# Kernel tuning notes

Hardware: AMD Instinct MI355X
Metric: run time of the kernel (lower is better)

The kernel has to match this reference:

```python
import jax, jax.numpy as jnp
import numpy as np

N = 100000   # nodes
E = 3200000  # edges
B = 64       # graphs in batch
NUM_CLASSES = 40


def _linear_params(key, out_c, in_c):
    k1, k2 = jax.random.split(key)
    bound = 1.0 / np.sqrt(in_c)
    W = jax.random.uniform(k1, (out_c, in_c), jnp.float32, -bound, bound)
    b = jax.random.uniform(k2, (out_c,), jnp.float32, -bound, bound)
    return W, b


def setup_inputs() -> dict:
    key = jax.random.key(0)
    ks = jax.random.split(key, 8)
    pos = jax.random.normal(ks[0], (N, 3), jnp.float32)
    edge_index = jax.random.randint(ks[1], (2, E), 0, N, dtype=jnp.int64)
    batch = jnp.sort(jax.random.randint(ks[2], (N,), 0, B, dtype=jnp.int64))
    # conv1 mlp: Linear(3+3 -> 32), Linear(32 -> 32)
    W11, b11 = _linear_params(ks[3], 32, 6)
    W12, b12 = _linear_params(ks[4], 32, 32)
    # conv2 mlp: Linear(32+3 -> 32), Linear(32 -> 32)
    W21, b21 = _linear_params(ks[5], 32, 35)
    W22, b22 = _linear_params(ks[6], 32, 32)
    # classifier: Linear(32 -> num_classes)
    Wc, bc = _linear_params(ks[7], NUM_CLASSES, 32)
    return {"pos": pos, "edge_index": edge_index, "batch": batch,
            "W11": W11, "b11": b11, "W12": W12, "b12": b12,
            "W21": W21, "b21": b21, "W22": W22, "b22": b22,
            "Wc": Wc, "bc": bc}


def _pointnet_layer(h, pos, src, dst, W1, b1, W2, b2):
    # message: concat(h_j, pos_j - pos_i) -> Linear -> ReLU -> Linear  per edge
    edge_feat = jnp.concatenate([h[src], pos[src] - pos[dst]], axis=-1)  # [E, C+3]
    m = jax.nn.relu(edge_feat @ W1.T + b1) @ W2.T + b2                   # [E, out]
    # aggr='max': scatter-max into target nodes; empty nodes -> 0
    agg = jax.ops.segment_max(m, dst, num_segments=N)
    return jnp.where(jnp.isneginf(agg), 0.0, agg)


def reference(pos, edge_index, batch, W11, b11, W12, b12, W21, b21, W22, b22, Wc, bc):
    src, dst = edge_index[0], edge_index[1]  # j (source), i (target)
    h = _pointnet_layer(pos, pos, src, dst, W11, b11, W12, b12)
    h = jax.nn.relu(h)
    h = _pointnet_layer(h, pos, src, dst, W21, b21, W22, b22)
    h = jax.nn.relu(h)
    g = jax.ops.segment_max(h, batch, num_segments=B)  # global_max_pool -> [B, 32]
    g = jnp.where(jnp.isneginf(g), 0.0, g)
    return g @ Wc.T + bc  # [B, num_classes]
```

## Files before the change

kernel.cpp:

```cpp
#include <hip/hip_runtime.h>

#define N_NODES 100000
#define N_EDGES 3200000
#define N_B 64
#define N_CLS 40
#define SCAN_NBLK 98
#define CAP 96

__global__ __launch_bounds__(256) void node1_kernel(
    const float* __restrict__ pos, const float* __restrict__ W11,
    const float* __restrict__ b11, float* __restrict__ A, float* __restrict__ C) {
  int n = blockIdx.x * 256 + threadIdx.x;
  if (n >= N_NODES) return;
  float p0 = pos[n * 3 + 0], p1 = pos[n * 3 + 1], p2 = pos[n * 3 + 2];
#pragma unroll
  for (int c = 0; c < 32; ++c) {
    float wa0 = W11[c * 6 + 0], wa1 = W11[c * 6 + 1], wa2 = W11[c * 6 + 2];
    float wp0 = W11[c * 6 + 3], wp1 = W11[c * 6 + 4], wp2 = W11[c * 6 + 5];
    float cp = p0 * wp0 + p1 * wp1 + p2 * wp2;
    A[(size_t)n * 32 + c] = p0 * wa0 + p1 * wa1 + p2 * wa2 + cp + b11[c];
    C[(size_t)n * 32 + c] = -cp;
  }
}

__global__ __launch_bounds__(256) void node2_kernel(
    const float* __restrict__ h1, const float* __restrict__ pos,
    const float* __restrict__ W21, const float* __restrict__ b21,
    float* __restrict__ A, float* __restrict__ C) {
  __shared__ float Wl[32 * 35];
  __shared__ float bl[32];
  for (int i = threadIdx.x; i < 32 * 35; i += 256) Wl[i] = W21[i];
  if (threadIdx.x < 32) bl[threadIdx.x] = b21[threadIdx.x];
  __syncthreads();

  int n = blockIdx.x * 256 + threadIdx.x;
  if (n >= N_NODES) return;

  float h[32];
  const float4* hp = reinterpret_cast<const float4*>(h1 + (size_t)n * 32);
#pragma unroll
  for (int q = 0; q < 8; ++q) {
    float4 v = hp[q];
    h[4 * q + 0] = v.x; h[4 * q + 1] = v.y;
    h[4 * q + 2] = v.z; h[4 * q + 3] = v.w;
  }
  float p0 = pos[n * 3 + 0], p1 = pos[n * 3 + 1], p2 = pos[n * 3 + 2];
#pragma unroll 4
  for (int co = 0; co < 32; ++co) {
    const float* wr = Wl + co * 35;
    float acc = bl[co];
#pragma unroll
    for (int k = 0; k < 32; ++k) acc = fmaf(h[k], wr[k], acc);
    float cp = p0 * wr[32] + p1 * wr[33] + p2 * wr[34];
    A[(size_t)n * 32 + co] = acc + cp;
    C[(size_t)n * 32 + co] = -cp;
  }
}

__global__ __launch_bounds__(256) void pscatter_kernel(
    const int* __restrict__ ei, int* __restrict__ cnt, int* __restrict__ slot) {
  int e = blockIdx.x * 256 + threadIdx.x;
  int s = ei[e];
  int d = ei[N_EDGES + e];
  int p = atomicAdd(cnt + d, 1);
  if (p < CAP) slot[d * CAP + p] = s;
}

__global__ __launch_bounds__(1024) void scan1_kernel(
    const int* __restrict__ cnt, int* __restrict__ offsets,
    int* __restrict__ bsum) {
  __shared__ int wsum[16];
  int i = blockIdx.x * 1024 + threadIdx.x;
  int lane = threadIdx.x & 63, wid = threadIdx.x >> 6;
  int v = (i < N_NODES) ? cnt[i] : 0;
  int x = v;
#pragma unroll
  for (int off = 1; off < 64; off <<= 1) {
    int t = __shfl_up(x, off, 64);
    if (lane >= off) x += t;
  }
  if (lane == 63) wsum[wid] = x;
  __syncthreads();
  if (wid == 0) {
    int s = (lane < 16) ? wsum[lane] : 0;
#pragma unroll
    for (int off = 1; off < 16; off <<= 1) {
      int t = __shfl_up(s, off, 64);
      if (lane >= off) s += t;
    }
    if (lane < 16) wsum[lane] = s;
  }
  __syncthreads();
  int excl = x - v + ((wid > 0) ? wsum[wid - 1] : 0);
  if (i < N_NODES) offsets[i] = excl;
  if (threadIdx.x == 0) bsum[blockIdx.x] = wsum[15];
}

__global__ __launch_bounds__(128) void scan2_kernel(int* __restrict__ bsum) {
  __shared__ int wtot[2];
  int i = threadIdx.x;
  int lane = i & 63, wid = i >> 6;
  int v = (i < SCAN_NBLK) ? bsum[i] : 0;
  int x = v;
#pragma unroll
  for (int off = 1; off < 64; off <<= 1) {
    int t = __shfl_up(x, off, 64);
    if (lane >= off) x += t;
  }
  if (lane == 63) wtot[wid] = x;
  __syncthreads();
  int excl = x - v + ((wid > 0) ? wtot[0] : 0);
  if (i < SCAN_NBLK) bsum[i] = excl;
}

__global__ __launch_bounds__(1024) void scan3_kernel(
    int* __restrict__ offsets, const int* __restrict__ bsum) {
  int i = blockIdx.x * 1024 + threadIdx.x;
  if (i < N_NODES) offsets[i] += bsum[blockIdx.x];
  if (blockIdx.x == 0 && threadIdx.x == 0) offsets[N_NODES] = N_EDGES;
}

__global__ __launch_bounds__(256) void compact_kernel(
    const int* __restrict__ offsets, const int* __restrict__ slot,
    int* __restrict__ ssrc, int* __restrict__ sdst) {
  int n = blockIdx.x * 256 + threadIdx.x;
  if (n >= N_NODES) return;
  int j0 = offsets[n];
  int deg = offsets[n + 1] - j0;
  if (deg > CAP) deg = CAP;
  const int* sp = slot + (size_t)n * CAP;
  for (int j = 0; j < deg; ++j) {
    ssrc[j0 + j] = sp[j];
    sdst[j0 + j] = n;
  }
}

__global__ __launch_bounds__(256) void edge_mlp_kernel(
    const int* __restrict__ ssrc, const int* __restrict__ sdst,
    const float* __restrict__ A, const float* __restrict__ C,
    const float* __restrict__ W2, const float* __restrict__ b2,
    unsigned* __restrict__ h) {
  __shared__ float Tm[256 * 33];
  __shared__ float Wl[1024];
  __shared__ float bl32[32];
  __shared__ short segstart[258];
  __shared__ int segdst[256];
  __shared__ int wh[4];
  __shared__ int nseg_s;

  int t = threadIdx.x;
  for (int i = t; i < 1024; i += 256) Wl[i] = W2[i];
  if (t < 32) bl32[t] = b2[t];

  int e = blockIdx.x * 256 + t;
  int s = ssrc[e];
  int d = sdst[e];
  int dprev = (e > 0) ? sdst[e - 1] : -1;
  bool head = (t == 0) || (d != dprev);

  unsigned long long mask = __ballot(head);
  int lane = t & 63, wid = t >> 6;
  if (lane == 63) wh[wid] = __popcll(mask);
  __syncthreads();
  int base = 0;
#pragma unroll
  for (int w = 0; w < 3; ++w) base += (w < wid) ? wh[w] : 0;
  int segid = base + __popcll(mask & ((2ULL << lane) - 1)) - 1;
  if (head) { segstart[segid] = (short)t; segdst[segid] = d; }
  if (t == 255) { nseg_s = segid + 1; segstart[segid + 1] = 256; }

  float r[32];
  const float4* Ap = reinterpret_cast<const float4*>(A + (size_t)s * 32);
  const float4* Cp = reinterpret_cast<const float4*>(C + (size_t)d * 32);
#pragma unroll
  for (int q = 0; q < 8; ++q) {
    float4 a = Ap[q];
    float4 c = Cp[q];
    r[4 * q + 0] = fmaxf(a.x + c.x, 0.f);
    r[4 * q + 1] = fmaxf(a.y + c.y, 0.f);
    r[4 * q + 2] = fmaxf(a.z + c.z, 0.f);
    r[4 * q + 3] = fmaxf(a.w + c.w, 0.f);
  }
#pragma unroll
  for (int co = 0; co < 32; ++co) {
    const float4* wr = reinterpret_cast<const float4*>(Wl + co * 32);
    float m = bl32[co];
#pragma unroll
    for (int q = 0; q < 8; ++q) {
      float4 w = wr[q];
      m = fmaf(r[4 * q + 0], w.x, m);
      m = fmaf(r[4 * q + 1], w.y, m);
      m = fmaf(r[4 * q + 2], w.z, m);
      m = fmaf(r[4 * q + 3], w.w, m);
    }
    Tm[t * 33 + co] = fmaxf(m, 0.f);
  }
  __syncthreads();

  int nseg = nseg_s;
  int c = t & 31;
  int e0 = blockIdx.x * 256;
  for (int sg = t >> 5; sg < nseg; sg += 8) {
    int j0 = segstart[sg], j1 = segstart[sg + 1];
    float v = 0.f;
    for (int j = j0; j < j1; ++j) v = fmaxf(v, Tm[j * 33 + c]);
    int dd = segdst[sg];
    bool contL = (j0 == 0) && (e0 > 0) && (sdst[e0 - 1] == dd);
    bool contR = (j1 == 256) && (e0 + 256 < N_EDGES) && (sdst[e0 + 256] == dd);
    unsigned* hp = h + (size_t)dd * 32 + c;
    if (contL || contR) atomicMax(hp, __float_as_uint(v));
    else *hp = __float_as_uint(v);
  }
}

__global__ __launch_bounds__(256) void pool_cls_kernel(
    const float* __restrict__ h2, const int* __restrict__ batch,
    const float* __restrict__ Wc, const float* __restrict__ bc,
    float* __restrict__ out) {
  int b = blockIdx.x;
  int lo = 0, hi = N_NODES;
  while (lo < hi) { int mid = (lo + hi) >> 1; if (batch[mid] < b) lo = mid + 1; else hi = mid; }
  int s = lo;
  hi = N_NODES;
  while (lo < hi) { int mid = (lo + hi) >> 1; if (batch[mid] < b + 1) lo = mid + 1; else hi = mid; }
  int e = lo;

  __shared__ float gl[8][32];
  int c = threadIdx.x & 31;
  int chunk = threadIdx.x >> 5;
  float m = 0.f;
  for (int n = s + chunk; n < e; n += 8) m = fmaxf(m, h2[(size_t)n * 32 + c]);
  gl[chunk][c] = m;
  __syncthreads();
  if (chunk == 0) {
    float v = gl[0][c];
#pragma unroll
    for (int q = 1; q < 8; ++q) v = fmaxf(v, gl[q][c]);
    gl[0][c] = v;
  }
  __syncthreads();
  if (threadIdx.x < N_CLS) {
    float accv = bc[threadIdx.x];
#pragma unroll
    for (int k = 0; k < 32; ++k) accv = fmaf(gl[0][k], Wc[threadIdx.x * 32 + k], accv);
    out[b * N_CLS + threadIdx.x] = accv;
  }
}

extern "C" void kernel_launch(void* const* d_in, const int* in_sizes, int n_in,
                              void* d_out, int out_size, void* d_ws, size_t ws_size,
                              hipStream_t stream) {
  const float* pos = (const float*)d_in[0];
  const int* ei    = (const int*)d_in[1];
  const int* batch = (const int*)d_in[2];
  const float* W11 = (const float*)d_in[3];
  const float* b11 = (const float*)d_in[4];
  const float* W12 = (const float*)d_in[5];
  const float* b12 = (const float*)d_in[6];
  const float* W21 = (const float*)d_in[7];
  const float* b21 = (const float*)d_in[8];
  const float* W22 = (const float*)d_in[9];
  const float* b22 = (const float*)d_in[10];
  const float* Wc  = (const float*)d_in[11];
  const float* bc  = (const float*)d_in[12];
  float* out = (float*)d_out;

  float* ws = (float*)d_ws;
  float* A = ws;
  float* C = ws + 3200000;
  float* h = ws + 6400000;
  int* slot = (int*)ws;
  int* ib      = (int*)(ws + 9600000);
  int* ssrc    = ib;
  int* sdst    = ib + N_EDGES;
  int* cnt     = ib + 2 * N_EDGES;
  int* offsets = ib + 2 * N_EDGES + N_NODES;
  int* bsum    = ib + 2 * N_EDGES + 2 * N_NODES + 1;

  int nb_nodes = (N_NODES + 255) / 256;
  int nb_edges = N_EDGES / 256;

  hipMemsetAsync(cnt, 0, (size_t)N_NODES * sizeof(int), stream);
  pscatter_kernel<<<nb_edges, 256, 0, stream>>>(ei, cnt, slot);
  scan1_kernel<<<SCAN_NBLK, 1024, 0, stream>>>(cnt, offsets, bsum);
  scan2_kernel<<<1, 128, 0, stream>>>(bsum);
  scan3_kernel<<<SCAN_NBLK, 1024, 0, stream>>>(offsets, bsum);
  compact_kernel<<<nb_nodes, 256, 0, stream>>>(offsets, slot, ssrc, sdst);

  node1_kernel<<<nb_nodes, 256, 0, stream>>>(pos, W11, b11, A, C);
  hipMemsetAsync(h, 0, (size_t)N_NODES * 32 * sizeof(float), stream);
  edge_mlp_kernel<<<nb_edges, 256, 0, stream>>>(ssrc, sdst, A, C, W12, b12, (unsigned*)h);
  node2_kernel<<<nb_nodes, 256, 0, stream>>>(h, pos, W21, b21, A, C);
  hipMemsetAsync(h, 0, (size_t)N_NODES * 32 * sizeof(float), stream);
  edge_mlp_kernel<<<nb_edges, 256, 0, stream>>>(ssrc, sdst, A, C, W22, b22, (unsigned*)h);
  pool_cls_kernel<<<N_B, 256, 0, stream>>>(h, batch, Wc, bc, out);
}
```

Baseline: 822.7 us.

## Restructure edge MLP: register-resident weights, fp16 shared staging of activations

The second per-edge linear layer is reorganised so each thread keeps 4 output channels' weights in registers and loops over 32 edges read from shared memory, instead of each thread computing all 32 outputs for its own edge with weights read from shared memory. Hidden activations and outputs are staged in shared memory as fp16, which halves LDS footprint and traffic and may raise occupancy. In exchange it adds an extra barrier and fp16 rounding of intermediate activations, which loses precision relative to the fp32 reference.

```diff
diff --git a/kernel.cpp b/kernel.cpp
--- a/kernel.cpp
+++ b/kernel.cpp
@@ -1,4 +1,5 @@
 #include <hip/hip_runtime.h>
+#include <hip/hip_fp16.h>
 
 #define N_NODES 100000
 #define N_EDGES 3200000
@@ -140,17 +141,29 @@
     const float* __restrict__ A, const float* __restrict__ C,
     const float* __restrict__ W2, const float* __restrict__ b2,
     unsigned* __restrict__ h) {
-  __shared__ float Tm[256 * 33];
-  __shared__ float Wl[1024];
-  __shared__ float bl32[32];
+  __shared__ __align__(16) __half Rr[256][40];
+  __shared__ __align__(16) __half Tm[256][40];
   __shared__ short segstart[258];
   __shared__ int segdst[256];
   __shared__ int wh[4];
   __shared__ int nseg_s;
 
   int t = threadIdx.x;
-  for (int i = t; i < 1024; i += 256) Wl[i] = W2[i];
-  if (t < 32) bl32[t] = b2[t];
+  int s0 = t & 31, cg = t >> 5;
+
+  float wreg[4][32];
+  float bl4[4];
+#pragma unroll
+  for (int i = 0; i < 4; ++i) {
+    const float4* wrow = reinterpret_cast<const float4*>(W2 + (cg * 4 + i) * 32);
+#pragma unroll
+    for (int q = 0; q < 8; ++q) {
+      float4 w = wrow[q];
+      wreg[i][4 * q + 0] = w.x; wreg[i][4 * q + 1] = w.y;
+      wreg[i][4 * q + 2] = w.z; wreg[i][4 * q + 3] = w.w;
+    }
+    bl4[i] = b2[cg * 4 + i];
+  }
 
   int e = blockIdx.x * 256 + t;
   int s = ssrc[e];
@@ -169,31 +182,51 @@
   if (head) { segstart[segid] = (short)t; segdst[segid] = d; }
   if (t == 255) { nseg_s = segid + 1; segstart[segid + 1] = 256; }
 
-  float r[32];
-  const float4* Ap = reinterpret_cast<const float4*>(A + (size_t)s * 32);
-  const float4* Cp = reinterpret_cast<const float4*>(C + (size_t)d * 32);
-#pragma unroll
-  for (int q = 0; q < 8; ++q) {
-    float4 a = Ap[q];
-    float4 c = Cp[q];
-    r[4 * q + 0] = fmaxf(a.x + c.x, 0.f);
-    r[4 * q + 1] = fmaxf(a.y + c.y, 0.f);
-    r[4 * q + 2] = fmaxf(a.z + c.z, 0.f);
-    r[4 * q + 3] = fmaxf(a.w + c.w, 0.f);
-  }
-#pragma unroll
-  for (int co = 0; co < 32; ++co) {
-    const float4* wr = reinterpret_cast<const float4*>(Wl + co * 32);
-    float m = bl32[co];
+  {
+    float r[32];
+    const float4* Ap = reinterpret_cast<const float4*>(A + (size_t)s * 32);
+    const float4* Cp = reinterpret_cast<const float4*>(C + (size_t)d * 32);
 #pragma unroll
     for (int q = 0; q < 8; ++q) {
-      float4 w = wr[q];
-      m = fmaf(r[4 * q + 0], w.x, m);
-      m = fmaf(r[4 * q + 1], w.y, m);
-      m = fmaf(r[4 * q + 2], w.z, m);
-      m = fmaf(r[4 * q + 3], w.w, m);
+      float4 a = Ap[q];
+      float4 c = Cp[q];
+      r[4 * q + 0] = fmaxf(a.x + c.x, 0.f);
+      r[4 * q + 1] = fmaxf(a.y + c.y, 0.f);
+      r[4 * q + 2] = fmaxf(a.z + c.z, 0.f);
+      r[4 * q + 3] = fmaxf(a.w + c.w, 0.f);
     }
-    Tm[t * 33 + co] = fmaxf(m, 0.f);
+    __half2 hh[16];
+#pragma unroll
+    for (int q = 0; q < 16; ++q) hh[q] = __floats2half2_rn(r[2 * q], r[2 * q + 1]);
+    float4* dst = reinterpret_cast<float4*>(&Rr[t][0]);
+    const float4* hsrc = reinterpret_cast<const float4*>(hh);
+#pragma unroll
+    for (int q = 0; q < 4; ++q) dst[q] = hsrc[q];
+  }
+  __syncthreads();
+
+#pragma unroll 2
+  for (int it = 0; it < 8; ++it) {
+    int ee = it * 32 + s0;
+    float4 vv[4];
+    const float4* rp = reinterpret_cast<const float4*>(&Rr[ee][0]);
+#pragma unroll
+    for (int q = 0; q < 4; ++q) vv[q] = rp[q];
+    const __half2* hp = reinterpret_cast<const __half2*>(vv);
+    float acc0 = bl4[0], acc1 = bl4[1], acc2 = bl4[2], acc3 = bl4[3];
+#pragma unroll
+    for (int q = 0; q < 16; ++q) {
+      float2 f = __half22float2(hp[q]);
+      acc0 = fmaf(f.x, wreg[0][2 * q], acc0); acc0 = fmaf(f.y, wreg[0][2 * q + 1], acc0);
+      acc1 = fmaf(f.x, wreg[1][2 * q], acc1); acc1 = fmaf(f.y, wreg[1][2 * q + 1], acc1);
+      acc2 = fmaf(f.x, wreg[2][2 * q], acc2); acc2 = fmaf(f.y, wreg[2][2 * q + 1], acc2);
+      acc3 = fmaf(f.x, wreg[3][2 * q], acc3); acc3 = fmaf(f.y, wreg[3][2 * q + 1], acc3);
+    }
+    __half2 o0 = __floats2half2_rn(fmaxf(acc0, 0.f), fmaxf(acc1, 0.f));
+    __half2 o1 = __floats2half2_rn(fmaxf(acc2, 0.f), fmaxf(acc3, 0.f));
+    __half2* tp = reinterpret_cast<__half2*>(&Tm[ee][0]);
+    tp[cg * 2 + 0] = o0;
+    tp[cg * 2 + 1] = o1;
   }
   __syncthreads();
 
@@ -203,13 +236,13 @@
   for (int sg = t >> 5; sg < nseg; sg += 8) {
     int j0 = segstart[sg], j1 = segstart[sg + 1];
     float v = 0.f;
-    for (int j = j0; j < j1; ++j) v = fmaxf(v, Tm[j * 33 + c]);
+    for (int j = j0; j < j1; ++j) v = fmaxf(v, __half2float(Tm[j][c]));
     int dd = segdst[sg];
     bool contL = (j0 == 0) && (e0 > 0) && (sdst[e0 - 1] == dd);
     bool contR = (j1 == 256) && (e0 + 256 < N_EDGES) && (sdst[e0 + 256] == dd);
-    unsigned* hp = h + (size_t)dd * 32 + c;
-    if (contL || contR) atomicMax(hp, __float_as_uint(v));
-    else *hp = __float_as_uint(v);
+    unsigned* hp2 = h + (size_t)dd * 32 + c;
+    if (contL || contR) atomicMax(hp2, __float_as_uint(v));
+    else *hp2 = __float_as_uint(v);
   }
 }
 
```

Result: slower. 962.8 us (+17.0%).
